# Kernel optimization log

Hardware: AMD Instinct MI355X
Metric: run time of the kernel (lower is better)

The kernel has to match this reference:

```python
import jax, jax.numpy as jnp
import numpy as np

CLUSTERS = 128
ITERATIONS = 10
TOPK = 32
NEG = -1e7


def setup_inputs() -> dict:
    key = jax.random.key(0)
    k1, k2, k3, k4 = jax.random.split(key, 4)
    N, L, H, E = 2, 2048, 8, 64
    BITS = 32
    return {
        "queries": jax.random.normal(k1, (N, L, H, E), dtype=jnp.float32),
        "keys": jax.random.normal(k2, (N, L, H, E), dtype=jnp.float32),
        "values": jax.random.normal(k3, (N, L, H, E), dtype=jnp.float32),
        "planes": jax.random.normal(k4, (BITS, E + 1), dtype=jnp.float32),
    }


def _cluster(bits, C, iterations):
    # bits: [N,H,L,B] in {0,1}. Lloyd k-means under Hamming distance.
    N, H, L, B = bits.shape
    init_idx = (np.arange(C) * L) // C
    cent = bits[:, :, init_idx, :]  # [N,H,C,B]
    for _ in range(iterations):
        # hamming(b,c) = b.(1-c) + (1-b).c
        d = (jnp.einsum('nhlb,nhcb->nhlc', bits, 1.0 - cent)
             + jnp.einsum('nhlb,nhcb->nhlc', 1.0 - bits, cent))
        assign = jnp.argmin(d, axis=-1)                      # [N,H,L]
        oh = jax.nn.one_hot(assign, C, dtype=jnp.float32)    # [N,H,L,C]
        cnt = oh.sum(axis=2)                                 # [N,H,C]
        sums = jnp.einsum('nhlc,nhlb->nhcb', oh, bits)
        new = (sums / jnp.maximum(cnt, 1.0)[..., None] >= 0.5).astype(jnp.float32)
        cent = jnp.where((cnt > 0.0)[..., None], new, cent)
    d = (jnp.einsum('nhlb,nhcb->nhlc', bits, 1.0 - cent)
         + jnp.einsum('nhlb,nhcb->nhlc', 1.0 - bits, cent))
    assign = jnp.argmin(d, axis=-1)
    oh = jax.nn.one_hot(assign, C, dtype=jnp.float32)
    cnt = oh.sum(axis=2)
    return assign, oh, cnt


def _forward(queries, keys, values, planes):
    # to [N,H,L,E]
    Q = jnp.transpose(queries, (0, 2, 1, 3))
    K = jnp.transpose(keys, (0, 2, 1, 3))
    V = jnp.transpose(values, (0, 2, 1, 3))
    N, H, L, E = Q.shape
    S = K.shape[2]
    temp = 1.0 / np.sqrt(E)

    # --- hash queries with random hyperplanes (bias column: hash_bias=True) ---
    x = jnp.concatenate([Q, jnp.ones(Q.shape[:-1] + (1,), Q.dtype)], axis=-1)
    bits = (jnp.einsum('nhle,be->nhlb', x, planes) > 0).astype(jnp.float32)

    # --- cluster queries (Lloyd on hamming distance over hash bits) ---
    assign, oh, cnt = _cluster(bits, CLUSTERS, ITERATIONS)

    # --- per-cluster centroid queries (mean over members) ---
    Qg = jnp.einsum('nhlc,nhle->nhce', oh, Q) / jnp.maximum(cnt, 1.0)[..., None]

    # --- top-k keys per cluster ---
    QKc = jnp.einsum('nhce,nhse->nhcs', Qg, K)   # [N,H,C,S]
    k = min(TOPK, S)
    _, tki = jax.lax.top_k(QKc, k)               # [N,H,C,k]

    # broadcast each cluster's top-k indices to its member queries
    idx_q = jnp.take_along_axis(
        tki, jnp.broadcast_to(assign[:, :, :, None], (N, H, L, k)), axis=2)  # [N,H,L,k]

    gather = jax.vmap(jax.vmap(lambda a, i: a[i]))
    K_sel = gather(K, idx_q)                     # [N,H,L,k,E]
    V_sel = gather(V, idx_q)                     # [N,H,L,k,E]

    qk = jnp.einsum('nhle,nhlke->nhlk', Q, K_sel)
    future = idx_q > jnp.arange(L)[None, None, :, None]   # causal: key pos > query pos
    qk = jnp.where(future, NEG, qk)
    A = jax.nn.softmax(temp * qk, axis=-1)
    A = A * (1.0 - future.astype(A.dtype))
    out = jnp.einsum('nhlk,nhlkd->nhld', A, V_sel)
    return jnp.transpose(out, (0, 2, 1, 3))      # [N,L,H,D]


def reference(queries, keys, values, planes):
    return _forward(queries, keys, values, planes)
```

## Files before the change

kernel.cpp:

```cpp
#include <hip/hip_runtime.h>
#include <math.h>

#define NB 2
#define HB 8
#define LB 2048
#define EB 64
#define BITSN 32
#define CLN 128
#define ITERS 10
#define TOPKN 32
#define NEGV -10000000.0f

typedef unsigned long long u64;
typedef unsigned int u32;

#define PART_NH16 (33 * 64)
#define PART_ITER16 (NB * HB * PART_NH16)
#define PART_TOTAL16 (ITERS * PART_ITER16)
#define BITS_BLOCKS 4096
#define ZBLOCKS ((PART_TOTAL16 + 255) / 256)

__global__ __launch_bounds__(256) void bits_zero_kernel(const float* __restrict__ q,
                                                        const float* __restrict__ planes,
                                                        u32* __restrict__ bits,
                                                        u32* __restrict__ zbuf) {
    int tid = threadIdx.x;
    int bid = blockIdx.x;
    if (bid >= BITS_BLOCKS) {
        int i = (bid - BITS_BLOCKS) * 256 + tid;
        if (i < PART_TOTAL16) zbuf[i] = 0u;
        return;
    }
    int wave = tid >> 6;
    int lane = tid & 63;
    int b = lane & 31;
    int which = lane >> 5;
    int qi = bid * 8 + wave * 2 + which;
    int l = qi & (LB - 1);
    int nh = qi / LB;
    int h = nh & (HB - 1);
    int n = nh / HB;
    const float* qrow = q + (((long long)n * LB + l) * HB + h) * EB;
    const float* prow = planes + b * (EB + 1);
    double acc = (double)prow[EB];
    #pragma unroll 8
    for (int e = 0; e < EB; ++e) acc += (double)qrow[e] * (double)prow[e];
    unsigned long long m = __ballot(acc > 0.0);
    if (b == 0) {
        bits[qi] = (u32)(which ? (m >> 32) : (m & 0xffffffffULL));
    }
}

__global__ __launch_bounds__(256) void kmeans_iter_kernel(const u32* __restrict__ bits,
                                                          const u32* __restrict__ part_prev,
                                                          u32* __restrict__ part_cur,
                                                          const u32* __restrict__ cent_prev_g,
                                                          u32* __restrict__ cent_cur_g,
                                                          int it) {
    __shared__ u32 cent[CLN];
    __shared__ int hist[33 * 128];
    int tid = threadIdx.x;
    int bid = blockIdx.x;
    int nh = bid >> 3;
    int tile = bid & 7;
    int lane = tid & 63;

    for (int i = tid; i < 33 * 128; i += 256) hist[i] = 0;
    if (tid < CLN) {
        u32 cv;
        if (it == 0) {
            cv = bits[nh * LB + tid * (LB / CLN)];
        } else {
            const u32* pp = part_prev + nh * PART_NH16;
            int sh = (tid & 1) * 16;
            int cnt = (int)((pp[32 * 64 + (tid >> 1)] >> sh) & 0xffffu);
            u32 nb = 0u;
            #pragma unroll
            for (int j = 0; j < BITSN; ++j) {
                int s = (int)((pp[j * 64 + (tid >> 1)] >> sh) & 0xffffu);
                if (2 * s >= cnt) nb |= (1u << j);
            }
            cv = (cnt > 0) ? nb : cent_prev_g[nh * CLN + tid];
        }
        cent[tid] = cv;
        if (tile == 0) cent_cur_g[nh * CLN + tid] = cv;
    }
    __syncthreads();

    int l = tile * 256 + tid;
    u32 bv = bits[nh * LB + l];

    u32 clo = cent[lane], chi = cent[lane + 64];
    u32 best = 0x7fffffffu;
    #pragma unroll 16
    for (int c = 0; c < 64; ++c) {
        u32 cc = (u32)__builtin_amdgcn_readlane((int)clo, c);
        u32 key = ((u32)__popc(bv ^ cc) << 7) | (u32)c;
        best = (key < best) ? key : best;
    }
    #pragma unroll 16
    for (int c = 0; c < 64; ++c) {
        u32 cc = (u32)__builtin_amdgcn_readlane((int)chi, c);
        u32 key = ((u32)__popc(bv ^ cc) << 7) | (u32)(64 + c);
        best = (key < best) ? key : best;
    }
    int bc = (int)(best & 127u);

    atomicAdd(&hist[32 * 128 + bc], 1);
    u32 bb = bv;
    while (bb) { int j = __ffs(bb) - 1; atomicAdd(&hist[j * 128 + bc], 1); bb &= bb - 1; }
    __syncthreads();

    u32* pc = part_cur + nh * PART_NH16;
    for (int i = tid; i < PART_NH16; i += 256) {
        int j = i >> 6, p = i & 63;
        u32 v = (u32)hist[j * 128 + 2 * p] | ((u32)hist[j * 128 + 2 * p + 1] << 16);
        if (v) atomicAdd(&pc[i], v);
    }
}

__global__ __launch_bounds__(1024) void list_final_kernel(const u32* __restrict__ bits,
                                                          const u32* __restrict__ part_prev,
                                                          const u32* __restrict__ cent_prev_g,
                                                          int* __restrict__ csort_g,
                                                          int* __restrict__ cnt_g,
                                                          int* __restrict__ ofs_g,
                                                          int* __restrict__ list_g) {
    __shared__ u32 cent[CLN];
    __shared__ int cnt[CLN];
    __shared__ int cntw[2][16][CLN];
    __shared__ int ofs[CLN];
    int nh = blockIdx.x;
    int tid = threadIdx.x;
    int w = tid >> 6, lane = tid & 63;

    if (tid < CLN) {
        const u32* pp = part_prev + nh * PART_NH16;
        int sh = (tid & 1) * 16;
        int cn = (int)((pp[32 * 64 + (tid >> 1)] >> sh) & 0xffffu);
        u32 nb = 0u;
        #pragma unroll
        for (int j = 0; j < BITSN; ++j) {
            int s = (int)((pp[j * 64 + (tid >> 1)] >> sh) & 0xffffu);
            if (2 * s >= cn) nb |= (1u << j);
        }
        cent[tid] = (cn > 0) ? nb : cent_prev_g[nh * CLN + tid];
        cnt[tid] = 0;
    }
    for (int i = tid; i < 2 * 16 * CLN; i += 1024) (&cntw[0][0][0])[i] = 0;
    __syncthreads();

    int l0 = tid, l1 = tid + 1024;
    u32 bv0 = bits[nh * LB + l0];
    u32 bv1 = bits[nh * LB + l1];
    u32 clo = cent[lane], chi = cent[lane + 64];
    u32 best0 = 0x7fffffffu, best1 = 0x7fffffffu;
    #pragma unroll 16
    for (int c = 0; c < 64; ++c) {
        u32 cc = (u32)__builtin_amdgcn_readlane((int)clo, c);
        u32 k0 = ((u32)__popc(bv0 ^ cc) << 7) | (u32)c;
        u32 k1 = ((u32)__popc(bv1 ^ cc) << 7) | (u32)c;
        best0 = (k0 < best0) ? k0 : best0;
        best1 = (k1 < best1) ? k1 : best1;
    }
    #pragma unroll 16
    for (int c = 0; c < 64; ++c) {
        u32 cc = (u32)__builtin_amdgcn_readlane((int)chi, c);
        u32 k0 = ((u32)__popc(bv0 ^ cc) << 7) | (u32)(64 + c);
        u32 k1 = ((u32)__popc(bv1 ^ cc) << 7) | (u32)(64 + c);
        best0 = (k0 < best0) ? k0 : best0;
        best1 = (k1 < best1) ? k1 : best1;
    }
    int bc0 = (int)(best0 & 127u);
    int bc1 = (int)(best1 & 127u);
    u64 ltmask = (lane == 0) ? 0ULL : (~0ULL >> (64 - lane));

    int rank0 = 0, rank1 = 0;
    for (int c = 0; c < CLN; ++c) {
        u64 m0 = __ballot(bc0 == c);
        u64 m1 = __ballot(bc1 == c);
        if ((m0 | m1) == 0ULL) continue;
        if (bc0 == c) rank0 = (int)__popcll(m0 & ltmask);
        if (bc1 == c) rank1 = (int)__popcll(m1 & ltmask);
        if (lane == 0) {
            int p0 = (int)__popcll(m0), p1 = (int)__popcll(m1);
            if (p0) cntw[0][w][c] = p0;
            if (p1) cntw[1][w][c] = p1;
            atomicAdd(&cnt[c], p0 + p1);
        }
    }
    __syncthreads();
    if (tid == 0) {
        int run = 0;
        for (int c = 0; c < CLN; ++c) { ofs[c] = run; run += cnt[c]; }
    }
    __syncthreads();
    if (tid < CLN) {
        int c = tid;
        int run = ofs[c];
        #pragma unroll
        for (int g = 0; g < 2; ++g)
            for (int ww = 0; ww < 16; ++ww) {
                int t = cntw[g][ww][c];
                cntw[g][ww][c] = run;
                run += t;
            }
        cnt_g[nh * CLN + c] = cnt[c];
        ofs_g[nh * CLN + c] = ofs[c];
    }
    __syncthreads();
    {
        int p0 = cntw[0][w][bc0] + rank0;
        int p1 = cntw[1][w][bc1] + rank1;
        list_g[nh * LB + p0] = l0;
        list_g[nh * LB + p1] = l1;
        csort_g[nh * LB + p0] = bc0;
        csort_g[nh * LB + p1] = bc1;
    }
}

__global__ __launch_bounds__(256) void qg_kernel(const float* __restrict__ q,
                                                 const int* __restrict__ cnt_g,
                                                 const int* __restrict__ ofs_g,
                                                 const int* __restrict__ list_g,
                                                 float* __restrict__ qgf) {
    __shared__ double ps[4][EB];
    int bid = blockIdx.x;
    int nh = bid >> 7;
    int h = nh & (HB - 1);
    int n = nh / HB;
    int tid = threadIdx.x;
    int w = tid >> 6, lane = tid & 63;
    int cn = cnt_g[bid];
    int o = ofs_g[bid];
    const int* lp = list_g + nh * LB + o;
    double acc = 0.0;
    for (int i = w; i < cn; i += 4) {
        int l = lp[i];
        acc += (double)q[(((long long)n * LB + l) * HB + h) * EB + lane];
    }
    ps[w][lane] = acc;
    __syncthreads();
    if (tid < EB) {
        double s = ((ps[0][tid] + ps[1][tid]) + ps[2][tid]) + ps[3][tid];
        double dcn = (double)(cn > 0 ? cn : 1);
        qgf[(long long)bid * EB + tid] = (float)(s / dcn);
    }
}

__global__ __launch_bounds__(256) void scores_kernel(const float* __restrict__ kk,
                                                     const float* __restrict__ qgf,
                                                     u32* __restrict__ keys) {
    __shared__ float qs[CLN * EB];
    int bid = blockIdx.x;
    int nh = bid >> 5;
    int tile = bid & 31;
    int h = nh & (HB - 1);
    int n = nh / HB;
    int tid = threadIdx.x;
    int w = tid >> 6;
    int lane = tid & 63;
    int l = tile * 64 + lane;
    int cbase = w * 32;

    {
        const float4* src = (const float4*)(qgf + (long long)nh * CLN * EB);
        float4* dst = (float4*)qs;
        #pragma unroll
        for (int i = 0; i < 8; ++i) dst[tid + 256 * i] = src[tid + 256 * i];
    }

    const float4* kr4 = (const float4*)(kk + (((long long)n * LB + l) * HB + h) * EB);
    float rr[EB];
    #pragma unroll
    for (int i = 0; i < 16; ++i) {
        float4 t4 = kr4[i];
        rr[4 * i] = t4.x; rr[4 * i + 1] = t4.y; rr[4 * i + 2] = t4.z; rr[4 * i + 3] = t4.w;
    }
    __syncthreads();

    for (int c = 0; c < 32; ++c) {
        const float4* qp = (const float4*)(qs + (cbase + c) * EB);
        float a0 = 0.f, a1 = 0.f, a2 = 0.f, a3 = 0.f;
        #pragma unroll
        for (int i = 0; i < 4; ++i) {
            float4 q0 = qp[i], q1 = qp[4 + i], q2 = qp[8 + i], q3 = qp[12 + i];
            int e0 = 4 * i, e1 = 16 + 4 * i, e2 = 32 + 4 * i, e3 = 48 + 4 * i;
            a0 = fmaf(q0.x, rr[e0], a0); a0 = fmaf(q0.y, rr[e0 + 1], a0);
            a0 = fmaf(q0.z, rr[e0 + 2], a0); a0 = fmaf(q0.w, rr[e0 + 3], a0);
            a1 = fmaf(q1.x, rr[e1], a1); a1 = fmaf(q1.y, rr[e1 + 1], a1);
            a1 = fmaf(q1.z, rr[e1 + 2], a1); a1 = fmaf(q1.w, rr[e1 + 3], a1);
            a2 = fmaf(q2.x, rr[e2], a2); a2 = fmaf(q2.y, rr[e2 + 1], a2);
            a2 = fmaf(q2.z, rr[e2 + 2], a2); a2 = fmaf(q2.w, rr[e2 + 3], a2);
            a3 = fmaf(q3.x, rr[e3], a3); a3 = fmaf(q3.y, rr[e3 + 1], a3);
            a3 = fmaf(q3.z, rr[e3 + 2], a3); a3 = fmaf(q3.w, rr[e3 + 3], a3);
        }
        float acc = (a0 + a1) + (a2 + a3);
        u32 u = __float_as_uint(acc);
        u = ((int)u < 0) ? ~u : (u | 0x80000000u);
        keys[((long long)(nh * CLN + cbase + c)) * LB + l] = u;
    }
}

__global__ __launch_bounds__(64) void topsel_kernel(const u32* __restrict__ keys,
                                                    int* __restrict__ tki_g) {
    int bid = blockIdx.x;
    int lane = threadIdx.x;
    const uint4* kp4 = (const uint4*)(keys + (long long)bid * LB);
    u64 k[32];
    #pragma unroll
    for (int t = 0; t < 8; ++t) {
        uint4 kv = kp4[lane + 64 * t];
        int l0 = (lane + 64 * t) * 4;
        k[4 * t]     = ((u64)kv.x << 32) | (u32)(2047 - l0);
        k[4 * t + 1] = ((u64)kv.y << 32) | (u32)(2047 - (l0 + 1));
        k[4 * t + 2] = ((u64)kv.z << 32) | (u32)(2047 - (l0 + 2));
        k[4 * t + 3] = ((u64)kv.w << 32) | (u32)(2047 - (l0 + 3));
    }
    u64 m0 = k[0], m1 = k[8], m2 = k[16], m3 = k[24];
    #pragma unroll
    for (int t = 1; t < 8; ++t) {
        if (k[t] > m0) m0 = k[t];
        if (k[8 + t] > m1) m1 = k[8 + t];
        if (k[16 + t] > m2) m2 = k[16 + t];
        if (k[24 + t] > m3) m3 = k[24 + t];
    }
    if (m1 > m0) m0 = m1;
    if (m3 > m2) m2 = m3;
    u64 cur = (m2 > m0) ? m2 : m0;

    for (int r = 0; r < TOPKN; ++r) {
        u64 wk = cur;
        #pragma unroll
        for (int off = 1; off < 64; off <<= 1) {
            u64 o = __shfl_xor(wk, off);
            if (o > wk) wk = o;
        }
        if (lane == 0) tki_g[bid * TOPKN + r] = 2047 - (int)(wk & 2047u);
        if (wk == cur) {
            u64 nm = 0ULL;
            #pragma unroll
            for (int t = 0; t < 32; ++t) {
                u64 kt = k[t];
                u64 cand = (kt < wk) ? kt : 0ULL;
                if (cand > nm) nm = cand;
            }
            cur = nm;
        }
    }
}

__device__ __forceinline__ void attn_one(const float* __restrict__ q,
                                         const float* __restrict__ kk,
                                         const float* __restrict__ vv,
                                         int n, int h, int l,
                                         const int* __restrict__ krow,
                                         int lane, float* __restrict__ out) {
    int j = lane & 31, p = lane >> 5;
    int kidx = krow[j];
    const float* vbase = vv + ((long long)n * LB * HB + h) * EB;
    float vreg[TOPKN];
    #pragma unroll
    for (int jj = 0; jj < TOPKN; ++jj) {
        int kj = __shfl(kidx, jj);
        vreg[jj] = vbase[(long long)kj * (HB * EB) + lane];
    }
    const float4* q4 = (const float4*)(q + (((long long)n * LB + l) * HB + h) * EB) + p * 8;
    const float4* k4 = (const float4*)(kk + (((long long)n * LB + kidx) * HB + h) * EB) + p * 8;
    float part = 0.f;
    #pragma unroll
    for (int i = 0; i < 8; ++i) {
        float4 a = q4[i], b = k4[i];
        part += a.x * b.x + a.y * b.y + a.z * b.z + a.w * b.w;
    }
    float qlo = __shfl(part, j);
    float qhi = __shfl(part, j + 32);
    float qk = qlo + qhi;
    bool future = kidx > l;
    float logit = 0.125f * (future ? NEGV : qk);
    float m = logit;
    #pragma unroll
    for (int off = 16; off; off >>= 1) m = fmaxf(m, __shfl_xor(m, off));
    float ex = expf(logit - m);
    float ssum = ex;
    #pragma unroll
    for (int off = 16; off; off >>= 1) ssum += __shfl_xor(ssum, off);
    float a = future ? 0.f : ex / ssum;
    float oacc = 0.f;
    #pragma unroll
    for (int jj = 0; jj < TOPKN; ++jj) {
        float aj = __shfl(a, jj);
        oacc = fmaf(aj, vreg[jj], oacc);
    }
    out[(((long long)n * LB + l) * HB + h) * EB + lane] = oacc;
}

__device__ __forceinline__ void attn_pair_body(const float* __restrict__ q,
                                               const float* __restrict__ kk,
                                               const float* __restrict__ vv,
                                               int n, int h, int l0, int l1,
                                               const int* __restrict__ krow,
                                               int lane, float* __restrict__ out) {
    int j = lane & 31, p = lane >> 5;
    int kidx = krow[j];
    const float* vbase = vv + ((long long)n * LB * HB + h) * EB;
    float vreg[TOPKN];
    #pragma unroll
    for (int jj = 0; jj < TOPKN; ++jj) {
        int kj = __shfl(kidx, jj);
        vreg[jj] = vbase[(long long)kj * (HB * EB) + lane];
    }
    const float4* q40 = (const float4*)(q + (((long long)n * LB + l0) * HB + h) * EB) + p * 8;
    const float4* q41 = (const float4*)(q + (((long long)n * LB + l1) * HB + h) * EB) + p * 8;
    const float4* k4  = (const float4*)(kk + (((long long)n * LB + kidx) * HB + h) * EB) + p * 8;
    float part0 = 0.f, part1 = 0.f;
    #pragma unroll
    for (int i = 0; i < 8; ++i) {
        float4 b = k4[i];
        float4 a0 = q40[i], a1 = q41[i];
        part0 += a0.x * b.x + a0.y * b.y + a0.z * b.z + a0.w * b.w;
        part1 += a1.x * b.x + a1.y * b.y + a1.z * b.z + a1.w * b.w;
    }
    float qk0 = __shfl(part0, j) + __shfl(part0, j + 32);
    float qk1 = __shfl(part1, j) + __shfl(part1, j + 32);
    bool fut0 = kidx > l0, fut1 = kidx > l1;
    float lg0 = 0.125f * (fut0 ? NEGV : qk0);
    float lg1 = 0.125f * (fut1 ? NEGV : qk1);
    float m0 = lg0, m1 = lg1;
    #pragma unroll
    for (int off = 16; off; off >>= 1) {
        m0 = fmaxf(m0, __shfl_xor(m0, off));
        m1 = fmaxf(m1, __shfl_xor(m1, off));
    }
    float e0 = expf(lg0 - m0), e1 = expf(lg1 - m1);
    float s0 = e0, s1 = e1;
    #pragma unroll
    for (int off = 16; off; off >>= 1) {
        s0 += __shfl_xor(s0, off);
        s1 += __shfl_xor(s1, off);
    }
    float a0 = fut0 ? 0.f : e0 / s0;
    float a1 = fut1 ? 0.f : e1 / s1;
    float o0 = 0.f, o1 = 0.f;
    #pragma unroll
    for (int jj = 0; jj < TOPKN; ++jj) {
        float aj0 = __shfl(a0, jj);
        float aj1 = __shfl(a1, jj);
        o0 = fmaf(aj0, vreg[jj], o0);
        o1 = fmaf(aj1, vreg[jj], o1);
    }
    out[(((long long)n * LB + l0) * HB + h) * EB + lane] = o0;
    out[(((long long)n * LB + l1) * HB + h) * EB + lane] = o1;
}

__global__ __launch_bounds__(256) void attn_quad_kernel(const float* __restrict__ q,
                                                        const float* __restrict__ kk,
                                                        const float* __restrict__ vv,
                                                        const int* __restrict__ list_g,
                                                        const int* __restrict__ csort_g,
                                                        const int* __restrict__ tki_g,
                                                        float* __restrict__ out) {
    int tid = threadIdx.x;
    int wave = tid >> 6, lane = tid & 63;
    int idx = blockIdx.x * 4 + wave;
    int nh = idx >> 9;
    int qd = idx & 511;
    int pos = 4 * qd;
    int l0 = list_g[nh * LB + pos];
    int l1 = list_g[nh * LB + pos + 1];
    int l2 = list_g[nh * LB + pos + 2];
    int l3 = list_g[nh * LB + pos + 3];
    int c0 = csort_g[nh * LB + pos];
    int c1 = csort_g[nh * LB + pos + 1];
    int c2 = csort_g[nh * LB + pos + 2];
    int c3 = csort_g[nh * LB + pos + 3];
    int h = nh & (HB - 1);
    int n = nh / HB;

    if ((c0 != c1) | (c1 != c2) | (c2 != c3)) {
        if (c0 == c1) {
            attn_pair_body(q, kk, vv, n, h, l0, l1, tki_g + (nh * CLN + c0) * TOPKN, lane, out);
        } else {
            attn_one(q, kk, vv, n, h, l0, tki_g + (nh * CLN + c0) * TOPKN, lane, out);
            attn_one(q, kk, vv, n, h, l1, tki_g + (nh * CLN + c1) * TOPKN, lane, out);
        }
        if (c2 == c3) {
            attn_pair_body(q, kk, vv, n, h, l2, l3, tki_g + (nh * CLN + c2) * TOPKN, lane, out);
        } else {
            attn_one(q, kk, vv, n, h, l2, tki_g + (nh * CLN + c2) * TOPKN, lane, out);
            attn_one(q, kk, vv, n, h, l3, tki_g + (nh * CLN + c3) * TOPKN, lane, out);
        }
        return;
    }

    const int* krow = tki_g + (nh * CLN + c0) * TOPKN;
    int j = lane & 31, p = lane >> 5;
    int kidx = krow[j];
    const float* vbase = vv + ((long long)n * LB * HB + h) * EB;
    float vreg[TOPKN];
    #pragma unroll
    for (int jj = 0; jj < TOPKN; ++jj) {
        int kj = __shfl(kidx, jj);
        vreg[jj] = vbase[(long long)kj * (HB * EB) + lane];
    }

    const float4* q40 = (const float4*)(q + (((long long)n * LB + l0) * HB + h) * EB) + p * 8;
    const float4* q41 = (const float4*)(q + (((long long)n * LB + l1) * HB + h) * EB) + p * 8;
    const float4* q42 = (const float4*)(q + (((long long)n * LB + l2) * HB + h) * EB) + p * 8;
    const float4* q43 = (const float4*)(q + (((long long)n * LB + l3) * HB + h) * EB) + p * 8;
    const float4* k4  = (const float4*)(kk + (((long long)n * LB + kidx) * HB + h) * EB) + p * 8;
    float p0 = 0.f, p1 = 0.f, p2 = 0.f, p3 = 0.f;
    #pragma unroll
    for (int i = 0; i < 8; ++i) {
        float4 b = k4[i];
        float4 a0 = q40[i], a1 = q41[i], a2 = q42[i], a3 = q43[i];
        p0 += a0.x * b.x + a0.y * b.y + a0.z * b.z + a0.w * b.w;
        p1 += a1.x * b.x + a1.y * b.y + a1.z * b.z + a1.w * b.w;
        p2 += a2.x * b.x + a2.y * b.y + a2.z * b.z + a2.w * b.w;
        p3 += a3.x * b.x + a3.y * b.y + a3.z * b.z + a3.w * b.w;
    }
    float qk0 = __shfl(p0, j) + __shfl(p0, j + 32);
    float qk1 = __shfl(p1, j) + __shfl(p1, j + 32);
    float qk2 = __shfl(p2, j) + __shfl(p2, j + 32);
    float qk3 = __shfl(p3, j) + __shfl(p3, j + 32);

    bool f0 = kidx > l0, f1 = kidx > l1, f2 = kidx > l2, f3 = kidx > l3;
    float g0 = 0.125f * (f0 ? NEGV : qk0);
    float g1 = 0.125f * (f1 ? NEGV : qk1);
    float g2 = 0.125f * (f2 ? NEGV : qk2);
    float g3 = 0.125f * (f3 ? NEGV : qk3);
    float m0 = g0, m1 = g1, m2 = g2, m3 = g3;
    #pragma unroll
    for (int off = 16; off; off >>= 1) {
        m0 = fmaxf(m0, __shfl_xor(m0, off));
        m1 = fmaxf(m1, __shfl_xor(m1, off));
        m2 = fmaxf(m2, __shfl_xor(m2, off));
        m3 = fmaxf(m3, __shfl_xor(m3, off));
    }
    float e0 = expf(g0 - m0), e1 = expf(g1 - m1);
    float e2 = expf(g2 - m2), e3 = expf(g3 - m3);
    float s0 = e0, s1 = e1, s2 = e2, s3 = e3;
    #pragma unroll
    for (int off = 16; off; off >>= 1) {
        s0 += __shfl_xor(s0, off);
        s1 += __shfl_xor(s1, off);
        s2 += __shfl_xor(s2, off);
        s3 += __shfl_xor(s3, off);
    }
    float a0 = f0 ? 0.f : e0 / s0;
    float a1 = f1 ? 0.f : e1 / s1;
    float a2 = f2 ? 0.f : e2 / s2;
    float a3 = f3 ? 0.f : e3 / s3;

    float o0 = 0.f, o1 = 0.f, o2 = 0.f, o3 = 0.f;
    #pragma unroll
    for (int jj = 0; jj < TOPKN; ++jj) {
        float v = vreg[jj];
        o0 = fmaf(__shfl(a0, jj), v, o0);
        o1 = fmaf(__shfl(a1, jj), v, o1);
        o2 = fmaf(__shfl(a2, jj), v, o2);
        o3 = fmaf(__shfl(a3, jj), v, o3);
    }
    out[(((long long)n * LB + l0) * HB + h) * EB + lane] = o0;
    out[(((long long)n * LB + l1) * HB + h) * EB + lane] = o1;
    out[(((long long)n * LB + l2) * HB + h) * EB + lane] = o2;
    out[(((long long)n * LB + l3) * HB + h) * EB + lane] = o3;
}

extern "C" void kernel_launch(void* const* d_in, const int* in_sizes, int n_in,
                              void* d_out, int out_size, void* d_ws, size_t ws_size,
                              hipStream_t stream) {
    const float* q = (const float*)d_in[0];
    const float* k = (const float*)d_in[1];
    const float* v = (const float*)d_in[2];
    const float* planes = (const float*)d_in[3];
    float* out = (float*)d_out;

    const int NQ = NB * HB * LB;
    char* ws = (char*)d_ws;
    u32* bits     = (u32*)(ws);
    int* csort_g  = (int*)(ws + 0x20000);
    int* cnt_g    = (int*)(ws + 0x40000);
    int* ofs_g    = (int*)(ws + 0x42000);
    int* list_g   = (int*)(ws + 0x44000);
    float* qgf    = (float*)(ws + 0x64000);
    int* tki_g    = (int*)(ws + 0xE4000);
    u32* keys     = (u32*)(ws + 0x124000);
    u32* part_all = (u32*)(ws + 0x124000);
    u32* cents0   = (u32*)(ws + 0x124000 + 0x180000);
    u32* cents1   = (u32*)(ws + 0x124000 + 0x182000);

    bits_zero_kernel<<<BITS_BLOCKS + ZBLOCKS, 256, 0, stream>>>(q, planes, bits, part_all);

    for (int it = 0; it < ITERS; ++it) {
        const u32* pp = part_all + (it == 0 ? 0 : (it - 1)) * PART_ITER16;
        u32* pc       = part_all + it * PART_ITER16;
        const u32* cprev = (it & 1) ? cents0 : cents1;
        u32* ccur        = (it & 1) ? cents1 : cents0;
        kmeans_iter_kernel<<<NB * HB * 8, 256, 0, stream>>>(bits, pp, pc, cprev, ccur, it);
    }
    list_final_kernel<<<NB * HB, 1024, 0, stream>>>(
        bits, part_all + 9 * PART_ITER16, cents1, csort_g, cnt_g, ofs_g, list_g);
    qg_kernel<<<NB * HB * CLN, 256, 0, stream>>>(q, cnt_g, ofs_g, list_g, qgf);
    scores_kernel<<<NB * HB * 32, 256, 0, stream>>>(k, qgf, keys);
    topsel_kernel<<<NB * HB * CLN, 64, 0, stream>>>(keys, tki_g);
    attn_quad_kernel<<<NQ / 16, 256, 0, stream>>>(q, k, v, list_g, csort_g, tki_g, out);
}
```

Before: 244.1 us.

## Replace iterative wave-max top-k selection with shared-memory bitonic sort

The top-k selection kernel now loads all 2048 packed score/index keys of a cluster row into shared memory and runs a full descending bitonic sort with 256 threads, then takes the first 32 entries. Before, a single 64-lane wave held 32 keys per lane in registers and did 32 rounds of shuffle-based max reduction. The change trades the serial per-round reductions for more parallel threads, at the cost of a full O(n log^2 n) sort with 66 block barriers and 16KB of shared memory per block.

```diff
diff --git a/kernel.cpp b/kernel.cpp
--- a/kernel.cpp
+++ b/kernel.cpp
@@ -302,52 +302,35 @@
     }
 }
 
-__global__ __launch_bounds__(64) void topsel_kernel(const u32* __restrict__ keys,
-                                                    int* __restrict__ tki_g) {
+__global__ __launch_bounds__(256) void topsel_kernel(const u32* __restrict__ keys,
+                                                     int* __restrict__ tki_g) {
+    __shared__ u64 sk[LB];
     int bid = blockIdx.x;
-    int lane = threadIdx.x;
-    const uint4* kp4 = (const uint4*)(keys + (long long)bid * LB);
-    u64 k[32];
+    int tid = threadIdx.x;
+    const u32* kp = keys + (long long)bid * LB;
     #pragma unroll
     for (int t = 0; t < 8; ++t) {
-        uint4 kv = kp4[lane + 64 * t];
-        int l0 = (lane + 64 * t) * 4;
-        k[4 * t]     = ((u64)kv.x << 32) | (u32)(2047 - l0);
-        k[4 * t + 1] = ((u64)kv.y << 32) | (u32)(2047 - (l0 + 1));
-        k[4 * t + 2] = ((u64)kv.z << 32) | (u32)(2047 - (l0 + 2));
-        k[4 * t + 3] = ((u64)kv.w << 32) | (u32)(2047 - (l0 + 3));
-    }
-    u64 m0 = k[0], m1 = k[8], m2 = k[16], m3 = k[24];
-    #pragma unroll
-    for (int t = 1; t < 8; ++t) {
-        if (k[t] > m0) m0 = k[t];
-        if (k[8 + t] > m1) m1 = k[8 + t];
-        if (k[16 + t] > m2) m2 = k[16 + t];
-        if (k[24 + t] > m3) m3 = k[24 + t];
-    }
-    if (m1 > m0) m0 = m1;
-    if (m3 > m2) m2 = m3;
-    u64 cur = (m2 > m0) ? m2 : m0;
-
-    for (int r = 0; r < TOPKN; ++r) {
-        u64 wk = cur;
-        #pragma unroll
-        for (int off = 1; off < 64; off <<= 1) {
-            u64 o = __shfl_xor(wk, off);
-            if (o > wk) wk = o;
-        }
-        if (lane == 0) tki_g[bid * TOPKN + r] = 2047 - (int)(wk & 2047u);
-        if (wk == cur) {
-            u64 nm = 0ULL;
+        int i = tid + 256 * t;
+        sk[i] = ((u64)kp[i] << 32) | (u32)(2047 - i);
+    }
+    __syncthreads();
+
+    for (int k = 2; k <= LB; k <<= 1) {
+        for (int j = k >> 1; j > 0; j >>= 1) {
             #pragma unroll
-            for (int t = 0; t < 32; ++t) {
-                u64 kt = k[t];
-                u64 cand = (kt < wk) ? kt : 0ULL;
-                if (cand > nm) nm = cand;
+            for (int t = 0; t < 8; ++t) {
+                int i = tid + 256 * t;
+                int ixj = i ^ j;
+                if (ixj > i) {
+                    u64 a = sk[i], b = sk[ixj];
+                    bool up = ((i & k) == 0);
+                    if (up ? (a < b) : (a > b)) { sk[i] = b; sk[ixj] = a; }
+                }
             }
-            cur = nm;
-        }
-    }
+            __syncthreads();
+        }
+    }
+    if (tid < TOPKN) tki_g[bid * TOPKN + tid] = 2047 - (int)(sk[tid] & 2047u);
 }
 
 __device__ __forceinline__ void attn_one(const float* __restrict__ q,
@@ -603,6 +586,6 @@
         bits, part_all + 9 * PART_ITER16, cents1, csort_g, cnt_g, ofs_g, list_g);
     qg_kernel<<<NB * HB * CLN, 256, 0, stream>>>(q, cnt_g, ofs_g, list_g, qgf);
     scores_kernel<<<NB * HB * 32, 256, 0, stream>>>(k, qgf, keys);
-    topsel_kernel<<<NB * HB * CLN, 64, 0, stream>>>(keys, tki_g);
+    topsel_kernel<<<NB * HB * CLN, 256, 0, stream>>>(keys, tki_g);
     attn_quad_kernel<<<NQ / 16, 256, 0, stream>>>(q, k, v, list_g, csort_g, tki_g, out);
 }
```

Result: slower. 337.7 us (+38.3%).

## Split top-k selection across four wavefronts with a shared-memory merge

Applied to the files above, without the earlier changes.

The top-32 selection per cluster row now uses 256 threads instead of one 64-lane wavefront. Each of four waves computes its local top-32 over a quarter of the 2048 scores. A single wave then merges the 128 candidates from shared memory into the final top-32. This shortens each wave's serial select-max chain and raises parallelism, at the cost of a block barrier and a second 32-round shuffle reduction.

```diff
diff --git a/kernel.cpp b/kernel.cpp
--- a/kernel.cpp
+++ b/kernel.cpp
@@ -302,50 +302,72 @@
     }
 }
 
-__global__ __launch_bounds__(64) void topsel_kernel(const u32* __restrict__ keys,
-                                                    int* __restrict__ tki_g) {
+__global__ __launch_bounds__(256) void topsel_kernel(const u32* __restrict__ keys,
+                                                     int* __restrict__ tki_g) {
+    __shared__ u64 cand[128];
     int bid = blockIdx.x;
-    int lane = threadIdx.x;
-    const uint4* kp4 = (const uint4*)(keys + (long long)bid * LB);
-    u64 k[32];
-    #pragma unroll
-    for (int t = 0; t < 8; ++t) {
-        uint4 kv = kp4[lane + 64 * t];
-        int l0 = (lane + 64 * t) * 4;
-        k[4 * t]     = ((u64)kv.x << 32) | (u32)(2047 - l0);
-        k[4 * t + 1] = ((u64)kv.y << 32) | (u32)(2047 - (l0 + 1));
-        k[4 * t + 2] = ((u64)kv.z << 32) | (u32)(2047 - (l0 + 2));
-        k[4 * t + 3] = ((u64)kv.w << 32) | (u32)(2047 - (l0 + 3));
-    }
-    u64 m0 = k[0], m1 = k[8], m2 = k[16], m3 = k[24];
-    #pragma unroll
-    for (int t = 1; t < 8; ++t) {
-        if (k[t] > m0) m0 = k[t];
-        if (k[8 + t] > m1) m1 = k[8 + t];
-        if (k[16 + t] > m2) m2 = k[16 + t];
-        if (k[24 + t] > m3) m3 = k[24 + t];
-    }
-    if (m1 > m0) m0 = m1;
-    if (m3 > m2) m2 = m3;
-    u64 cur = (m2 > m0) ? m2 : m0;
-
-    for (int r = 0; r < TOPKN; ++r) {
-        u64 wk = cur;
+    int tid = threadIdx.x;
+    int w = tid >> 6, lane = tid & 63;
+
+    {
+        const uint4* kp4 = (const uint4*)(keys + (long long)bid * LB);
+        u64 k[8];
         #pragma unroll
-        for (int off = 1; off < 64; off <<= 1) {
-            u64 o = __shfl_xor(wk, off);
-            if (o > wk) wk = o;
-        }
-        if (lane == 0) tki_g[bid * TOPKN + r] = 2047 - (int)(wk & 2047u);
-        if (wk == cur) {
-            u64 nm = 0ULL;
+        for (int t = 0; t < 2; ++t) {
+            int qi = w * 128 + lane + 64 * t;
+            uint4 kv = kp4[qi];
+            int l0 = qi * 4;
+            k[4 * t]     = ((u64)kv.x << 32) | (u32)(2047 - l0);
+            k[4 * t + 1] = ((u64)kv.y << 32) | (u32)(2047 - (l0 + 1));
+            k[4 * t + 2] = ((u64)kv.z << 32) | (u32)(2047 - (l0 + 2));
+            k[4 * t + 3] = ((u64)kv.w << 32) | (u32)(2047 - (l0 + 3));
+        }
+        u64 m0 = k[0], m1 = k[4];
+        #pragma unroll
+        for (int t = 1; t < 4; ++t) {
+            if (k[t] > m0) m0 = k[t];
+            if (k[4 + t] > m1) m1 = k[4 + t];
+        }
+        u64 cur = (m1 > m0) ? m1 : m0;
+
+        for (int r = 0; r < TOPKN; ++r) {
+            u64 wk = cur;
             #pragma unroll
-            for (int t = 0; t < 32; ++t) {
-                u64 kt = k[t];
-                u64 cand = (kt < wk) ? kt : 0ULL;
-                if (cand > nm) nm = cand;
+            for (int off = 1; off < 64; off <<= 1) {
+                u64 o = __shfl_xor(wk, off);
+                if (o > wk) wk = o;
             }
-            cur = nm;
+            if (lane == 0) cand[w * TOPKN + r] = wk;
+            if (wk == cur) {
+                u64 nm = 0ULL;
+                #pragma unroll
+                for (int t = 0; t < 8; ++t) {
+                    u64 kt = k[t];
+                    u64 c2 = (kt < wk) ? kt : 0ULL;
+                    if (c2 > nm) nm = c2;
+                }
+                cur = nm;
+            }
+        }
+    }
+    __syncthreads();
+
+    if (w == 0) {
+        u64 k0 = cand[lane], k1 = cand[lane + 64];
+        u64 cur = (k0 > k1) ? k0 : k1;
+        for (int r = 0; r < TOPKN; ++r) {
+            u64 wk = cur;
+            #pragma unroll
+            for (int off = 1; off < 64; off <<= 1) {
+                u64 o = __shfl_xor(wk, off);
+                if (o > wk) wk = o;
+            }
+            if (lane == 0) tki_g[bid * TOPKN + r] = 2047 - (int)(wk & 2047u);
+            if (wk == cur) {
+                u64 a = (k0 < wk) ? k0 : 0ULL;
+                u64 b = (k1 < wk) ? k1 : 0ULL;
+                cur = (a > b) ? a : b;
+            }
         }
     }
 }
@@ -603,6 +625,6 @@
         bits, part_all + 9 * PART_ITER16, cents1, csort_g, cnt_g, ofs_g, list_g);
     qg_kernel<<<NB * HB * CLN, 256, 0, stream>>>(q, cnt_g, ofs_g, list_g, qgf);
     scores_kernel<<<NB * HB * 32, 256, 0, stream>>>(k, qgf, keys);
-    topsel_kernel<<<NB * HB * CLN, 64, 0, stream>>>(keys, tki_g);
+    topsel_kernel<<<NB * HB * CLN, 256, 0, stream>>>(keys, tki_g);
     attn_quad_kernel<<<NQ / 16, 256, 0, stream>>>(q, k, v, list_g, csort_g, tki_g, out);
 }
```

Result: slower. 258.8 us (+6.0%).
